# Kernel tuning notes

Measured on AMD Instinct MI355X. Metric: run time of the kernel, lower is better.

The kernel has to match this reference:

```python
import jax, jax.numpy as jnp
import numpy as np

N_NODES = 50000
N_EDGES = 800000
N_GRAPHS = 512
HIDDEN = 256
NODE_FEAT = 9
LAYERS = 4


def setup_inputs() -> dict:
    key = jax.random.key(0)
    ks = jax.random.split(key, 9)
    x = jax.random.normal(ks[0], (N_NODES, NODE_FEAT), dtype=jnp.float32)
    edge_index = jax.random.randint(ks[1], (2, N_EDGES), 0, N_NODES, dtype=jnp.int64)
    batch = jnp.sort(jax.random.randint(ks[2], (N_NODES,), 0, N_GRAPHS, dtype=jnp.int64))
    embed_W = jax.random.normal(ks[3], (NODE_FEAT, HIDDEN), dtype=jnp.float32) * (1.0 / np.sqrt(NODE_FEAT))
    embed_b = jnp.zeros((HIDDEN,), dtype=jnp.float32)
    conv_W = jax.random.normal(ks[4], (LAYERS, HIDDEN, HIDDEN), dtype=jnp.float32) * (1.0 / np.sqrt(HIDDEN))
    conv_b = jnp.zeros((LAYERS, HIDDEN), dtype=jnp.float32)
    out_W = jax.random.normal(ks[5], (HIDDEN, 1), dtype=jnp.float32) * (1.0 / np.sqrt(HIDDEN))
    out_b = jnp.zeros((1,), dtype=jnp.float32)
    return {"x": x, "edge_index": edge_index, "batch": batch,
            "embed_W": embed_W, "embed_b": embed_b,
            "conv_W": conv_W, "conv_b": conv_b,
            "out_W": out_W, "out_b": out_b}


def reference(x, edge_index, batch, embed_W, embed_b, conv_W, conv_b, out_W, out_b):
    n = x.shape[0]
    src, dst = edge_index[0], edge_index[1]
    # GCN symmetric normalization with self-loops: deg includes the self-loop (+1)
    deg = jax.ops.segment_sum(jnp.ones(src.shape[0], x.dtype), dst, num_segments=n) + 1.0
    dinv = jax.lax.rsqrt(deg)                       # [N]
    norm_e = dinv[src] * dinv[dst]                  # [E] edge coefficient
    self_coef = (dinv * dinv)[:, None]              # [N,1] self-loop coefficient

    h = jax.nn.relu(x @ embed_W + embed_b)          # [N,H]
    for l in range(conv_W.shape[0]):
        hw = h @ conv_W[l]                          # [N,H] transform first
        msg = hw[src] * norm_e[:, None]             # [E,H] gather + scale
        agg = jax.ops.segment_sum(msg, dst, num_segments=n)  # scatter-add
        agg = agg + hw * self_coef                  # self-loop contribution
        h = jax.nn.relu(agg + conv_b[l])

    # global mean pool over graph ids
    sums = jax.ops.segment_sum(h, batch, num_segments=N_GRAPHS)           # [G,H]
    cnt = jax.ops.segment_sum(jnp.ones(n, h.dtype), batch, num_segments=N_GRAPHS)
    pooled = sums / jnp.maximum(cnt, 1.0)[:, None]
    return pooled @ out_W + out_b                   # [G,1]
```

## Files before the change

kernel.cpp:

```cpp
#include <hip/hip_runtime.h>

#define N_NODES 50000
#define N_EDGES 800000
#define N_GRAPHS 512
#define HIDDEN 256
#define NODE_FEAT 9
#define LAYERS 4
#define BUCKET 64

typedef float floatx4 __attribute__((ext_vector_type(4)));
typedef short short8 __attribute__((ext_vector_type(8)));
typedef unsigned uint2v __attribute__((ext_vector_type(2)));

__device__ __forceinline__ float bf2f(unsigned u) {
    unsigned v = u << 16;
    float f;
    __builtin_memcpy(&f, &v, 4);
    return f;
}
__device__ __forceinline__ unsigned short f2bf(float f) {
    unsigned v;
    __builtin_memcpy(&v, &f, 4);
    v += 0x7FFFu + ((v >> 16) & 1u);
    return (unsigned short)(v >> 16);
}

__global__ __launch_bounds__(256) void aux_kernel(const int* __restrict__ cnt,
                                                  float* __restrict__ dinv,
                                                  const int* __restrict__ batch,
                                                  int* __restrict__ gstart) {
    int i = blockIdx.x * 256 + threadIdx.x;
    if (i < N_NODES) dinv[i] = rsqrtf((float)(cnt[i] + 1));
    int g = i - N_NODES;
    if (g >= 0 && g <= N_GRAPHS) {
        if (g == N_GRAPHS) { gstart[g] = N_NODES; return; }
        int lo = 0, hi = N_NODES;
        while (lo < hi) {
            int mid = (lo + hi) >> 1;
            if (batch[mid] < g) lo = mid + 1; else hi = mid;
        }
        gstart[g] = lo;
    }
}

__global__ __launch_bounds__(256) void packW_kernel(const float* __restrict__ W,
                                                    unsigned short* __restrict__ Wsw) {
    int idx = blockIdx.x * 256 + threadIdx.x;
    int lane = idx & 63;
    int ct   = (idx >> 6) & 15;
    int ks   = (idx >> 10) & 7;
    int l    = idx >> 13;
    int n = ct * 16 + (lane & 15);
    int kbase = ks * 32 + (lane >> 4) * 8;
    const float* Wl = W + (size_t)l * HIDDEN * HIDDEN;
    alignas(16) unsigned short tmp[8];
    #pragma unroll
    for (int j = 0; j < 8; j++)
        tmp[j] = f2bf(Wl[(size_t)(kbase + j) * HIDDEN + n]);
    *(uint4*)&Wsw[(size_t)idx * 8] = *(const uint4*)tmp;
}

__global__ __launch_bounds__(256, 3) void embed_gemm(const float* __restrict__ x,
                                                     const float* __restrict__ embW,
                                                     const float* __restrict__ embb,
                                                     const unsigned short* __restrict__ Wsw,
                                                     unsigned short* __restrict__ hwout, int N,
                                                     const int* __restrict__ srcE,
                                                     const int* __restrict__ dstE,
                                                     int* __restrict__ cnt,
                                                     int* __restrict__ col_src) {
    __shared__ unsigned short As[64][264];
    int t = threadIdx.x;
    int wv = t >> 6, lane = t & 63, quad = lane >> 4, l15 = lane & 15;
    int n0 = blockIdx.x * 64;

    const short8* Wl = (const short8*)Wsw;
    short8 bq[2][4];
    #pragma unroll
    for (int ci = 0; ci < 4; ci++)
        bq[0][ci] = Wl[(size_t)(wv * 4 + ci) * 64 + lane];

    #pragma unroll 2
    for (int i = 0; i < 8; i++) {
        int j = t + i * 256;
        int r = j >> 5;
        int c8 = j & 31;
        int n = n0 + r;
        unsigned o0 = 0, o1 = 0, o2 = 0, o3 = 0;
        if (n < N) {
            float xr[NODE_FEAT];
            #pragma unroll
            for (int k = 0; k < NODE_FEAT; k++) xr[k] = x[(size_t)n * NODE_FEAT + k];
            float4 a0 = *(const float4*)&embb[c8 * 8];
            float4 a1 = *(const float4*)&embb[c8 * 8 + 4];
            #pragma unroll
            for (int k = 0; k < NODE_FEAT; k++) {
                float4 w0 = *(const float4*)&embW[k * HIDDEN + c8 * 8];
                float4 w1 = *(const float4*)&embW[k * HIDDEN + c8 * 8 + 4];
                a0.x += xr[k] * w0.x; a0.y += xr[k] * w0.y;
                a0.z += xr[k] * w0.z; a0.w += xr[k] * w0.w;
                a1.x += xr[k] * w1.x; a1.y += xr[k] * w1.y;
                a1.z += xr[k] * w1.z; a1.w += xr[k] * w1.w;
            }
            o0 = (unsigned)f2bf(fmaxf(a0.x, 0.f)) | ((unsigned)f2bf(fmaxf(a0.y, 0.f)) << 16);
            o1 = (unsigned)f2bf(fmaxf(a0.z, 0.f)) | ((unsigned)f2bf(fmaxf(a0.w, 0.f)) << 16);
            o2 = (unsigned)f2bf(fmaxf(a1.x, 0.f)) | ((unsigned)f2bf(fmaxf(a1.y, 0.f)) << 16);
            o3 = (unsigned)f2bf(fmaxf(a1.z, 0.f)) | ((unsigned)f2bf(fmaxf(a1.w, 0.f)) << 16);
        }
        *(uint4*)&As[r][c8 * 8] = make_uint4(o0, o1, o2, o3);
    }
    __syncthreads();

    floatx4 acc[4][4];
    #pragma unroll
    for (int i = 0; i < 4; i++)
        #pragma unroll
        for (int j = 0; j < 4; j++)
            acc[i][j] = (floatx4){0.f, 0.f, 0.f, 0.f};

    #pragma unroll
    for (int ks = 0; ks < 8; ks++) {
        if (ks < 7) {
            #pragma unroll
            for (int ci = 0; ci < 4; ci++)
                bq[(ks + 1) & 1][ci] = Wl[(size_t)((ks + 1) * 16 + wv * 4 + ci) * 64 + lane];
        }
        short8 a[4];
        #pragma unroll
        for (int rt = 0; rt < 4; rt++)
            a[rt] = *(const short8*)&As[rt * 16 + l15][ks * 32 + quad * 8];
        #pragma unroll
        for (int rt = 0; rt < 4; rt++)
            #pragma unroll
            for (int ci = 0; ci < 4; ci++)
                acc[rt][ci] = __builtin_amdgcn_mfma_f32_16x16x32_bf16(a[rt], bq[ks & 1][ci], acc[rt][ci], 0, 0, 0);
    }

    __syncthreads();
    #pragma unroll
    for (int rt = 0; rt < 4; rt++) {
        #pragma unroll
        for (int ci = 0; ci < 4; ci++) {
            int col = (wv * 4 + ci) * 16 + l15;
            int rowb = rt * 16 + quad * 4;
            #pragma unroll
            for (int reg = 0; reg < 4; reg++)
                As[rowb + reg][col] = f2bf(acc[rt][ci][reg]);
        }
    }
    __syncthreads();
    #pragma unroll
    for (int i = 0; i < 8; i++) {
        int j = t + i * 256;
        int r = j >> 5;
        int c = j & 31;
        int n = n0 + r;
        if (n < N)
            *(uint4*)&hwout[(size_t)n * HIDDEN + c * 8] = *(const uint4*)&As[r][c * 8];
    }

    int stride = gridDim.x * 256;
    for (int e = blockIdx.x * 256 + t; e < N_EDGES; e += stride) {
        int d = dstE[e];
        int pos = atomicAdd(&cnt[d], 1);
        if (pos < BUCKET) col_src[d * BUCKET + pos] = srcE[e];
    }
}

__global__ __launch_bounds__(256, 3) void gemm_mfma(const unsigned short* __restrict__ hin,
                                                    const unsigned short* __restrict__ Wsw,
                                                    unsigned short* __restrict__ hwout, int N) {
    __shared__ unsigned short As[64][264];
    int t = threadIdx.x;
    int wv = t >> 6, lane = t & 63, quad = lane >> 4, l15 = lane & 15;
    int n0 = blockIdx.x * 64;
    const uint4* h4 = (const uint4*)hin;

    uint4 av[8];
    #pragma unroll
    for (int i = 0; i < 8; i++) {
        int j = t + i * 256;
        int r = j >> 5;
        int c = j & 31;
        int n = n0 + r;
        av[i] = make_uint4(0u, 0u, 0u, 0u);
        if (n < N) av[i] = h4[(size_t)n * 32 + c];
    }
    const short8* Wl = (const short8*)Wsw;
    short8 bq[2][4];
    #pragma unroll
    for (int ci = 0; ci < 4; ci++)
        bq[0][ci] = Wl[(size_t)(wv * 4 + ci) * 64 + lane];
    #pragma unroll
    for (int i = 0; i < 8; i++) {
        int j = t + i * 256;
        int r = j >> 5;
        int c = j & 31;
        *(uint4*)&As[r][c * 8] = av[i];
    }
    __syncthreads();

    floatx4 acc[4][4];
    #pragma unroll
    for (int i = 0; i < 4; i++)
        #pragma unroll
        for (int j = 0; j < 4; j++)
            acc[i][j] = (floatx4){0.f, 0.f, 0.f, 0.f};

    #pragma unroll
    for (int ks = 0; ks < 8; ks++) {
        if (ks < 7) {
            #pragma unroll
            for (int ci = 0; ci < 4; ci++)
                bq[(ks + 1) & 1][ci] = Wl[(size_t)((ks + 1) * 16 + wv * 4 + ci) * 64 + lane];
        }
        short8 a[4];
        #pragma unroll
        for (int rt = 0; rt < 4; rt++)
            a[rt] = *(const short8*)&As[rt * 16 + l15][ks * 32 + quad * 8];
        #pragma unroll
        for (int rt = 0; rt < 4; rt++)
            #pragma unroll
            for (int ci = 0; ci < 4; ci++)
                acc[rt][ci] = __builtin_amdgcn_mfma_f32_16x16x32_bf16(a[rt], bq[ks & 1][ci], acc[rt][ci], 0, 0, 0);
    }

    __syncthreads();
    #pragma unroll
    for (int rt = 0; rt < 4; rt++) {
        #pragma unroll
        for (int ci = 0; ci < 4; ci++) {
            int col = (wv * 4 + ci) * 16 + l15;
            int rowb = rt * 16 + quad * 4;
            #pragma unroll
            for (int reg = 0; reg < 4; reg++)
                As[rowb + reg][col] = f2bf(acc[rt][ci][reg]);
        }
    }
    __syncthreads();
    #pragma unroll
    for (int i = 0; i < 8; i++) {
        int j = t + i * 256;
        int r = j >> 5;
        int c = j & 31;
        int n = n0 + r;
        if (n < N)
            *(uint4*)&hwout[(size_t)n * HIDDEN + c * 8] = *(const uint4*)&As[r][c * 8];
    }
}

__global__ __launch_bounds__(256) void agg_kernel(const unsigned short* __restrict__ hw,
                                                  const int* __restrict__ cnt,
                                                  const int* __restrict__ col_src,
                                                  const float* __restrict__ dinv,
                                                  const float* __restrict__ bias,
                                                  unsigned short* __restrict__ hout) {
    __shared__ uint2 sEdge[4][64];
    int wv = threadIdx.x >> 6, lane = threadIdx.x & 63;
    int n = blockIdx.x * 4 + wv;
    if (n >= N_NODES) return;
    float dn = dinv[n];
    int deg = cnt[n]; if (deg > BUCKET) deg = BUCKET;

    uint2 s2 = ((const uint2*)(hw + (size_t)n * HIDDEN))[lane];
    float4 b4 = *(const float4*)&bias[4 * lane];
    float selfc = dn * dn;
    float a0 = bf2f(s2.x & 0xFFFFu) * selfc + b4.x;
    float a1 = bf2f(s2.x >> 16)     * selfc + b4.y;
    float a2 = bf2f(s2.y & 0xFFFFu) * selfc + b4.z;
    float a3 = bf2f(s2.y >> 16)     * selfc + b4.w;

    if (lane < deg) {
        int s = col_src[n * BUCKET + lane];
        float nr = dinv[s] * dn;
        unsigned nrb;
        __builtin_memcpy(&nrb, &nr, 4);
        sEdge[wv][lane] = make_uint2((unsigned)s, nrb);
    }
    for (int i = 0; i < deg; i++) {
        uint2 p = sEdge[wv][i];
        float nr;
        __builtin_memcpy(&nr, &p.y, 4);
        uint2 u = ((const uint2*)(hw + (size_t)p.x * HIDDEN))[lane];
        a0 += nr * bf2f(u.x & 0xFFFFu);
        a1 += nr * bf2f(u.x >> 16);
        a2 += nr * bf2f(u.y & 0xFFFFu);
        a3 += nr * bf2f(u.y >> 16);
    }
    unsigned p0 = (unsigned)f2bf(fmaxf(a0, 0.0f)) | ((unsigned)f2bf(fmaxf(a1, 0.0f)) << 16);
    unsigned p1 = (unsigned)f2bf(fmaxf(a2, 0.0f)) | ((unsigned)f2bf(fmaxf(a3, 0.0f)) << 16);
    uint2v pv; pv.x = p0; pv.y = p1;
    __builtin_nontemporal_store(pv, (uint2v*)(hout + (size_t)n * HIDDEN) + lane);
}

__global__ __launch_bounds__(256) void agg_dot_kernel(const unsigned short* __restrict__ hw,
                                                      const int* __restrict__ cnt,
                                                      const int* __restrict__ col_src,
                                                      const float* __restrict__ dinv,
                                                      const float* __restrict__ bias,
                                                      const float* __restrict__ outW,
                                                      float* __restrict__ dotv) {
    __shared__ uint2 sEdge[4][64];
    int wv = threadIdx.x >> 6, lane = threadIdx.x & 63;
    int n = blockIdx.x * 4 + wv;
    if (n >= N_NODES) return;
    float dn = dinv[n];
    int deg = cnt[n]; if (deg > BUCKET) deg = BUCKET;

    uint2 s2 = ((const uint2*)(hw + (size_t)n * HIDDEN))[lane];
    float4 b4 = *(const float4*)&bias[4 * lane];
    float selfc = dn * dn;
    float a0 = bf2f(s2.x & 0xFFFFu) * selfc + b4.x;
    float a1 = bf2f(s2.x >> 16)     * selfc + b4.y;
    float a2 = bf2f(s2.y & 0xFFFFu) * selfc + b4.z;
    float a3 = bf2f(s2.y >> 16)     * selfc + b4.w;

    if (lane < deg) {
        int s = col_src[n * BUCKET + lane];
        float nr = dinv[s] * dn;
        unsigned nrb;
        __builtin_memcpy(&nrb, &nr, 4);
        sEdge[wv][lane] = make_uint2((unsigned)s, nrb);
    }
    for (int i = 0; i < deg; i++) {
        uint2 p = sEdge[wv][i];
        float nr;
        __builtin_memcpy(&nr, &p.y, 4);
        uint2 u = ((const uint2*)(hw + (size_t)p.x * HIDDEN))[lane];
        a0 += nr * bf2f(u.x & 0xFFFFu);
        a1 += nr * bf2f(u.x >> 16);
        a2 += nr * bf2f(u.y & 0xFFFFu);
        a3 += nr * bf2f(u.y >> 16);
    }
    float4 w = *(const float4*)&outW[4 * lane];
    float dot = fmaxf(a0, 0.0f) * w.x + fmaxf(a1, 0.0f) * w.y
              + fmaxf(a2, 0.0f) * w.z + fmaxf(a3, 0.0f) * w.w;
    #pragma unroll
    for (int off = 32; off > 0; off >>= 1) dot += __shfl_xor(dot, off, 64);
    if (lane == 0) dotv[n] = dot;
}

__global__ __launch_bounds__(64) void finalize_kernel(const float* __restrict__ dotv,
                                                      const int* __restrict__ gstart,
                                                      const float* __restrict__ outb,
                                                      float* __restrict__ out) {
    int g = blockIdx.x;
    int lane = threadIdx.x;
    int s = gstart[g], e = gstart[g + 1];
    float acc = 0.0f;
    for (int n = s + lane; n < e; n += 64) acc += dotv[n];
    #pragma unroll
    for (int off = 32; off > 0; off >>= 1) acc += __shfl_xor(acc, off, 64);
    if (lane == 0) out[g] = acc / fmaxf((float)(e - s), 1.0f) + outb[0];
}

extern "C" void kernel_launch(void* const* d_in, const int* in_sizes, int n_in,
                              void* d_out, int out_size, void* d_ws, size_t ws_size,
                              hipStream_t stream) {
    const float* x     = (const float*)d_in[0];
    const int*   edge  = (const int*)d_in[1];
    const int*   src   = edge;
    const int*   dst   = edge + N_EDGES;
    const int*   batch = (const int*)d_in[2];
    const float* embW  = (const float*)d_in[3];
    const float* embb  = (const float*)d_in[4];
    const float* convW = (const float*)d_in[5];
    const float* convb = (const float*)d_in[6];
    const float* outW  = (const float*)d_in[7];
    const float* outb  = (const float*)d_in[8];
    float* out = (float*)d_out;

    char* ws = (char*)d_ws;
    size_t off = 0;
    auto take = [&](size_t bytes) { char* p = ws + off; off += (bytes + 255) & ~(size_t)255; return p; };
    int*   cnt     = (int*)  take((size_t)N_NODES * 4);
    int*   col_src = (int*)  take((size_t)N_NODES * BUCKET * 4);
    float* dinv    = (float*)take((size_t)N_NODES * 4);
    int*   gstart  = (int*)  take((size_t)(N_GRAPHS + 1) * 4);
    float* dotv    = (float*)take((size_t)N_NODES * 4);
    unsigned short* Wsw = (unsigned short*)take((size_t)LAYERS * 8 * 16 * 64 * 8 * 2);
    unsigned short* h0  = (unsigned short*)take((size_t)N_NODES * HIDDEN * 2);
    unsigned short* h1  = (unsigned short*)take((size_t)N_NODES * HIDDEN * 2);

    hipMemsetAsync(cnt, 0, (size_t)N_NODES * 4, stream);

    packW_kernel<<<128, 256, 0, stream>>>(convW, Wsw);

    int nblk = (N_NODES + 63) / 64;
    int ablk = (N_NODES + 3) / 4;
    int xblk = (N_NODES + N_GRAPHS + 1 + 255) / 256;

    embed_gemm<<<nblk, 256, 0, stream>>>(x, embW, embb, Wsw, h1, N_NODES,
                                         src, dst, cnt, col_src);
    aux_kernel<<<xblk, 256, 0, stream>>>(cnt, dinv, batch, gstart);
    agg_kernel<<<ablk, 256, 0, stream>>>(h1, cnt, col_src, dinv, convb + 0 * HIDDEN, h0);
    gemm_mfma<<<nblk, 256, 0, stream>>>(h0, Wsw + (size_t)1 * 65536, h1, N_NODES);
    agg_kernel<<<ablk, 256, 0, stream>>>(h1, cnt, col_src, dinv, convb + 1 * HIDDEN, h0);
    gemm_mfma<<<nblk, 256, 0, stream>>>(h0, Wsw + (size_t)2 * 65536, h1, N_NODES);
    agg_kernel<<<ablk, 256, 0, stream>>>(h1, cnt, col_src, dinv, convb + 2 * HIDDEN, h0);
    gemm_mfma<<<nblk, 256, 0, stream>>>(h0, Wsw + (size_t)3 * 65536, h1, N_NODES);
    agg_dot_kernel<<<ablk, 256, 0, stream>>>(h1, cnt, col_src, dinv, convb + 3 * HIDDEN, outW, dotv);

    finalize_kernel<<<N_GRAPHS, 64, 0, stream>>>(dotv, gstart, outb, out);
}
```

Before: 465.9 us.

## Slice hidden features into column-sliced layout for cache-local aggregation gather

Stores the bf16 hidden activations in 8 column slices of 32 features each (slice-major), and reworks the aggregation kernels so each block handles one slice for 16 nodes, with 16 lanes per node. Each slice's working set (about 3.2 MB) is small enough to stay cache-resident during the random neighbour gathers, replacing full 512-byte row gathers across the whole 25 MB tensor. Bucket filling of edges moves out of the embedding GEMM into its own kernel. The final dot product becomes per-slice partials that the finalize kernel sums. This adds 8x more edge-list loads per node and shorter 64-byte-per-node gather segments. N_NODES/16 happens to be exact here.

```diff
diff --git a/kernel.cpp b/kernel.cpp
--- a/kernel.cpp
+++ b/kernel.cpp
@@ -7,10 +7,10 @@
 #define NODE_FEAT 9
 #define LAYERS 4
 #define BUCKET 64
+#define NSLICE 8
 
 typedef float floatx4 __attribute__((ext_vector_type(4)));
 typedef short short8 __attribute__((ext_vector_type(8)));
-typedef unsigned uint2v __attribute__((ext_vector_type(2)));
 
 __device__ __forceinline__ float bf2f(unsigned u) {
     unsigned v = u << 16;
@@ -23,6 +23,19 @@
     __builtin_memcpy(&v, &f, 4);
     v += 0x7FFFu + ((v >> 16) & 1u);
     return (unsigned short)(v >> 16);
+}
+__device__ __forceinline__ size_t smb(int s, int n) {
+    return ((size_t)s * N_NODES + (size_t)n) * 32;
+}
+
+__global__ void fillb_kernel(const int* __restrict__ src, const int* __restrict__ dst,
+                             int* __restrict__ cnt, int* __restrict__ col_src, int E) {
+    int e = blockIdx.x * blockDim.x + threadIdx.x;
+    if (e < E) {
+        int d = dst[e];
+        int pos = atomicAdd(&cnt[d], 1);
+        if (pos < BUCKET) col_src[d * BUCKET + pos] = src[e];
+    }
 }
 
 __global__ __launch_bounds__(256) void aux_kernel(const int* __restrict__ cnt,
@@ -64,11 +77,7 @@
                                                      const float* __restrict__ embW,
                                                      const float* __restrict__ embb,
                                                      const unsigned short* __restrict__ Wsw,
-                                                     unsigned short* __restrict__ hwout, int N,
-                                                     const int* __restrict__ srcE,
-                                                     const int* __restrict__ dstE,
-                                                     int* __restrict__ cnt,
-                                                     int* __restrict__ col_src) {
+                                                     unsigned short* __restrict__ hwout, int N) {
     __shared__ unsigned short As[64][264];
     int t = threadIdx.x;
     int wv = t >> 6, lane = t & 63, quad = lane >> 4, l15 = lane & 15;
@@ -156,14 +165,7 @@
         int c = j & 31;
         int n = n0 + r;
         if (n < N)
-            *(uint4*)&hwout[(size_t)n * HIDDEN + c * 8] = *(const uint4*)&As[r][c * 8];
-    }
-
-    int stride = gridDim.x * 256;
-    for (int e = blockIdx.x * 256 + t; e < N_EDGES; e += stride) {
-        int d = dstE[e];
-        int pos = atomicAdd(&cnt[d], 1);
-        if (pos < BUCKET) col_src[d * BUCKET + pos] = srcE[e];
+            *(uint4*)&hwout[smb(c >> 2, n) + (c & 3) * 8] = *(const uint4*)&As[r][c * 8];
     }
 }
 
@@ -174,7 +176,6 @@
     int t = threadIdx.x;
     int wv = t >> 6, lane = t & 63, quad = lane >> 4, l15 = lane & 15;
     int n0 = blockIdx.x * 64;
-    const uint4* h4 = (const uint4*)hin;
 
     uint4 av[8];
     #pragma unroll
@@ -184,7 +185,7 @@
         int c = j & 31;
         int n = n0 + r;
         av[i] = make_uint4(0u, 0u, 0u, 0u);
-        if (n < N) av[i] = h4[(size_t)n * 32 + c];
+        if (n < N) av[i] = *(const uint4*)&hin[smb(c >> 2, n) + (c & 3) * 8];
     }
     const short8* Wl = (const short8*)Wsw;
     short8 bq[2][4];
@@ -245,7 +246,7 @@
         int c = j & 31;
         int n = n0 + r;
         if (n < N)
-            *(uint4*)&hwout[(size_t)n * HIDDEN + c * 8] = *(const uint4*)&As[r][c * 8];
+            *(uint4*)&hwout[smb(c >> 2, n) + (c & 3) * 8] = *(const uint4*)&As[r][c * 8];
     }
 }
 
@@ -255,42 +256,44 @@
                                                   const float* __restrict__ dinv,
                                                   const float* __restrict__ bias,
                                                   unsigned short* __restrict__ hout) {
-    __shared__ uint2 sEdge[4][64];
-    int wv = threadIdx.x >> 6, lane = threadIdx.x & 63;
-    int n = blockIdx.x * 4 + wv;
-    if (n >= N_NODES) return;
+    __shared__ uint2 sEdge[4][4][BUCKET];
+    int t = threadIdx.x;
+    int wv = t >> 6, lane = t & 63;
+    int sub = lane >> 4, cl = lane & 15;
+    int slice = blockIdx.x & 7;
+    int chunk = blockIdx.x >> 3;
+    int n = chunk * 16 + wv * 4 + sub;
     float dn = dinv[n];
     int deg = cnt[n]; if (deg > BUCKET) deg = BUCKET;
 
-    uint2 s2 = ((const uint2*)(hw + (size_t)n * HIDDEN))[lane];
-    float4 b4 = *(const float4*)&bias[4 * lane];
+    #pragma unroll
+    for (int r = 0; r < 4; r++) {
+        int e = cl + r * 16;
+        if (e < deg) {
+            int s = col_src[n * BUCKET + e];
+            float nr = dinv[s] * dn;
+            unsigned nrb; __builtin_memcpy(&nrb, &nr, 4);
+            sEdge[wv][sub][e] = make_uint2((unsigned)s, nrb);
+        }
+    }
+
+    size_t sb = smb(slice, n);
+    unsigned su = *(const unsigned*)&hw[sb + 2 * cl];
+    float2 b2 = *(const float2*)&bias[slice * 32 + 2 * cl];
     float selfc = dn * dn;
-    float a0 = bf2f(s2.x & 0xFFFFu) * selfc + b4.x;
-    float a1 = bf2f(s2.x >> 16)     * selfc + b4.y;
-    float a2 = bf2f(s2.y & 0xFFFFu) * selfc + b4.z;
-    float a3 = bf2f(s2.y >> 16)     * selfc + b4.w;
-
-    if (lane < deg) {
-        int s = col_src[n * BUCKET + lane];
-        float nr = dinv[s] * dn;
-        unsigned nrb;
-        __builtin_memcpy(&nrb, &nr, 4);
-        sEdge[wv][lane] = make_uint2((unsigned)s, nrb);
-    }
+    float a0 = bf2f(su & 0xFFFFu) * selfc + b2.x;
+    float a1 = bf2f(su >> 16)     * selfc + b2.y;
+
+    size_t slice_base = (size_t)slice * N_NODES;
     for (int i = 0; i < deg; i++) {
-        uint2 p = sEdge[wv][i];
-        float nr;
-        __builtin_memcpy(&nr, &p.y, 4);
-        uint2 u = ((const uint2*)(hw + (size_t)p.x * HIDDEN))[lane];
-        a0 += nr * bf2f(u.x & 0xFFFFu);
-        a1 += nr * bf2f(u.x >> 16);
-        a2 += nr * bf2f(u.y & 0xFFFFu);
-        a3 += nr * bf2f(u.y >> 16);
-    }
-    unsigned p0 = (unsigned)f2bf(fmaxf(a0, 0.0f)) | ((unsigned)f2bf(fmaxf(a1, 0.0f)) << 16);
-    unsigned p1 = (unsigned)f2bf(fmaxf(a2, 0.0f)) | ((unsigned)f2bf(fmaxf(a3, 0.0f)) << 16);
-    uint2v pv; pv.x = p0; pv.y = p1;
-    __builtin_nontemporal_store(pv, (uint2v*)(hout + (size_t)n * HIDDEN) + lane);
+        uint2 p = sEdge[wv][sub][i];
+        float nr; __builtin_memcpy(&nr, &p.y, 4);
+        unsigned u = *(const unsigned*)&hw[(slice_base + p.x) * 32 + 2 * cl];
+        a0 += nr * bf2f(u & 0xFFFFu);
+        a1 += nr * bf2f(u >> 16);
+    }
+    unsigned o = (unsigned)f2bf(fmaxf(a0, 0.0f)) | ((unsigned)f2bf(fmaxf(a1, 0.0f)) << 16);
+    *(unsigned*)&hout[sb + 2 * cl] = o;
 }
 
 __global__ __launch_bounds__(256) void agg_dot_kernel(const unsigned short* __restrict__ hw,
@@ -299,48 +302,51 @@
                                                       const float* __restrict__ dinv,
                                                       const float* __restrict__ bias,
                                                       const float* __restrict__ outW,
-                                                      float* __restrict__ dotv) {
-    __shared__ uint2 sEdge[4][64];
-    int wv = threadIdx.x >> 6, lane = threadIdx.x & 63;
-    int n = blockIdx.x * 4 + wv;
-    if (n >= N_NODES) return;
+                                                      float* __restrict__ dotp) {
+    __shared__ uint2 sEdge[4][4][BUCKET];
+    int t = threadIdx.x;
+    int wv = t >> 6, lane = t & 63;
+    int sub = lane >> 4, cl = lane & 15;
+    int slice = blockIdx.x & 7;
+    int chunk = blockIdx.x >> 3;
+    int n = chunk * 16 + wv * 4 + sub;
     float dn = dinv[n];
     int deg = cnt[n]; if (deg > BUCKET) deg = BUCKET;
 
-    uint2 s2 = ((const uint2*)(hw + (size_t)n * HIDDEN))[lane];
-    float4 b4 = *(const float4*)&bias[4 * lane];
+    #pragma unroll
+    for (int r = 0; r < 4; r++) {
+        int e = cl + r * 16;
+        if (e < deg) {
+            int s = col_src[n * BUCKET + e];
+            float nr = dinv[s] * dn;
+            unsigned nrb; __builtin_memcpy(&nrb, &nr, 4);
+            sEdge[wv][sub][e] = make_uint2((unsigned)s, nrb);
+        }
+    }
+
+    size_t sb = smb(slice, n);
+    unsigned su = *(const unsigned*)&hw[sb + 2 * cl];
+    float2 b2 = *(const float2*)&bias[slice * 32 + 2 * cl];
     float selfc = dn * dn;
-    float a0 = bf2f(s2.x & 0xFFFFu) * selfc + b4.x;
-    float a1 = bf2f(s2.x >> 16)     * selfc + b4.y;
-    float a2 = bf2f(s2.y & 0xFFFFu) * selfc + b4.z;
-    float a3 = bf2f(s2.y >> 16)     * selfc + b4.w;
-
-    if (lane < deg) {
-        int s = col_src[n * BUCKET + lane];
-        float nr = dinv[s] * dn;
-        unsigned nrb;
-        __builtin_memcpy(&nrb, &nr, 4);
-        sEdge[wv][lane] = make_uint2((unsigned)s, nrb);
-    }
+    float a0 = bf2f(su & 0xFFFFu) * selfc + b2.x;
+    float a1 = bf2f(su >> 16)     * selfc + b2.y;
+
+    size_t slice_base = (size_t)slice * N_NODES;
     for (int i = 0; i < deg; i++) {
-        uint2 p = sEdge[wv][i];
-        float nr;
-        __builtin_memcpy(&nr, &p.y, 4);
-        uint2 u = ((const uint2*)(hw + (size_t)p.x * HIDDEN))[lane];
-        a0 += nr * bf2f(u.x & 0xFFFFu);
-        a1 += nr * bf2f(u.x >> 16);
-        a2 += nr * bf2f(u.y & 0xFFFFu);
-        a3 += nr * bf2f(u.y >> 16);
-    }
-    float4 w = *(const float4*)&outW[4 * lane];
-    float dot = fmaxf(a0, 0.0f) * w.x + fmaxf(a1, 0.0f) * w.y
-              + fmaxf(a2, 0.0f) * w.z + fmaxf(a3, 0.0f) * w.w;
-    #pragma unroll
-    for (int off = 32; off > 0; off >>= 1) dot += __shfl_xor(dot, off, 64);
-    if (lane == 0) dotv[n] = dot;
-}
-
-__global__ __launch_bounds__(64) void finalize_kernel(const float* __restrict__ dotv,
+        uint2 p = sEdge[wv][sub][i];
+        float nr; __builtin_memcpy(&nr, &p.y, 4);
+        unsigned u = *(const unsigned*)&hw[(slice_base + p.x) * 32 + 2 * cl];
+        a0 += nr * bf2f(u & 0xFFFFu);
+        a1 += nr * bf2f(u >> 16);
+    }
+    float2 w2 = *(const float2*)&outW[slice * 32 + 2 * cl];
+    float dot = fmaxf(a0, 0.0f) * w2.x + fmaxf(a1, 0.0f) * w2.y;
+    #pragma unroll
+    for (int off = 8; off > 0; off >>= 1) dot += __shfl_xor(dot, off, 64);
+    if (cl == 0) dotp[(size_t)n * NSLICE + slice] = dot;
+}
+
+__global__ __launch_bounds__(64) void finalize_kernel(const float* __restrict__ dotp,
                                                       const int* __restrict__ gstart,
                                                       const float* __restrict__ outb,
                                                       float* __restrict__ out) {
@@ -348,7 +354,7 @@
     int lane = threadIdx.x;
     int s = gstart[g], e = gstart[g + 1];
     float acc = 0.0f;
-    for (int n = s + lane; n < e; n += 64) acc += dotv[n];
+    for (size_t i = (size_t)s * NSLICE + lane; i < (size_t)e * NSLICE; i += 64) acc += dotp[i];
     #pragma unroll
     for (int off = 32; off > 0; off >>= 1) acc += __shfl_xor(acc, off, 64);
     if (lane == 0) out[g] = acc / fmaxf((float)(e - s), 1.0f) + outb[0];
@@ -377,7 +383,7 @@
     int*   col_src = (int*)  take((size_t)N_NODES * BUCKET * 4);
     float* dinv    = (float*)take((size_t)N_NODES * 4);
     int*   gstart  = (int*)  take((size_t)(N_GRAPHS + 1) * 4);
-    float* dotv    = (float*)take((size_t)N_NODES * 4);
+    float* dotp    = (float*)take((size_t)N_NODES * NSLICE * 4);
     unsigned short* Wsw = (unsigned short*)take((size_t)LAYERS * 8 * 16 * 64 * 8 * 2);
     unsigned short* h0  = (unsigned short*)take((size_t)N_NODES * HIDDEN * 2);
     unsigned short* h1  = (unsigned short*)take((size_t)N_NODES * HIDDEN * 2);
@@ -385,21 +391,20 @@
     hipMemsetAsync(cnt, 0, (size_t)N_NODES * 4, stream);
 
     packW_kernel<<<128, 256, 0, stream>>>(convW, Wsw);
+    fillb_kernel<<<(N_EDGES + 255) / 256, 256, 0, stream>>>(src, dst, cnt, col_src, N_EDGES);
+    aux_kernel<<<(N_NODES + N_GRAPHS + 1 + 255) / 256, 256, 0, stream>>>(cnt, dinv, batch, gstart);
 
     int nblk = (N_NODES + 63) / 64;
-    int ablk = (N_NODES + 3) / 4;
-    int xblk = (N_NODES + N_GRAPHS + 1 + 255) / 256;
-
-    embed_gemm<<<nblk, 256, 0, stream>>>(x, embW, embb, Wsw, h1, N_NODES,
-                                         src, dst, cnt, col_src);
-    aux_kernel<<<xblk, 256, 0, stream>>>(cnt, dinv, batch, gstart);
+    int ablk = (N_NODES / 16) * NSLICE;
+
+    embed_gemm<<<nblk, 256, 0, stream>>>(x, embW, embb, Wsw, h1, N_NODES);
     agg_kernel<<<ablk, 256, 0, stream>>>(h1, cnt, col_src, dinv, convb + 0 * HIDDEN, h0);
     gemm_mfma<<<nblk, 256, 0, stream>>>(h0, Wsw + (size_t)1 * 65536, h1, N_NODES);
     agg_kernel<<<ablk, 256, 0, stream>>>(h1, cnt, col_src, dinv, convb + 1 * HIDDEN, h0);
     gemm_mfma<<<nblk, 256, 0, stream>>>(h0, Wsw + (size_t)2 * 65536, h1, N_NODES);
     agg_kernel<<<ablk, 256, 0, stream>>>(h1, cnt, col_src, dinv, convb + 2 * HIDDEN, h0);
     gemm_mfma<<<nblk, 256, 0, stream>>>(h0, Wsw + (size_t)3 * 65536, h1, N_NODES);
-    agg_dot_kernel<<<ablk, 256, 0, stream>>>(h1, cnt, col_src, dinv, convb + 3 * HIDDEN, outW, dotv);
-
-    finalize_kernel<<<N_GRAPHS, 64, 0, stream>>>(dotv, gstart, outb, out);
-}
+    agg_dot_kernel<<<ablk, 256, 0, stream>>>(h1, cnt, col_src, dinv, convb + 3 * HIDDEN, outW, dotp);
+
+    finalize_kernel<<<N_GRAPHS, 64, 0, stream>>>(dotp, gstart, outb, out);
+}
```

New measurement: 518.3 us. 1.11x slower.
